# Optimization experiments

Hardware: AMD Instinct MI355X
Metric: run time of the kernel (lower is better)

## Reference

```python
import jax, jax.numpy as jnp
import numpy as np

TILE = 128
NEG = -1e10


def rotate_half(x):
    half = x.shape[-1] // 2
    return jnp.concatenate([-x[..., half:], x[..., :half]], axis=-1)


def setup_inputs() -> dict:
    key = jax.random.key(0)
    ks = jax.random.split(key, 7)
    B, S, E, H, D, K = 1, 4096, 2048, 16, 128, 8
    T = S // TILE
    x = jax.random.normal(ks[0], (B, S, E), jnp.float32)
    wq = jax.random.normal(ks[1], (E, H * D), jnp.float32) * 0.02
    wk = jax.random.normal(ks[2], (E, H * D), jnp.float32) * 0.02
    wv = jax.random.normal(ks[3], (E, H * D), jnp.float32) * 0.02
    wo = jax.random.normal(ks[4], (H * D, E), jnp.float32) * 0.02
    rope_angles = jax.random.uniform(ks[5], (S, D // 2), jnp.float32)
    anchor_indices = jax.random.randint(ks[6], (B, H, T, K), 0, T).astype(jnp.int32)
    return {"x": x, "wq": wq, "wk": wk, "wv": wv, "wo": wo,
            "rope_angles": rope_angles, "anchor_indices": anchor_indices}


def reference(x, wq, wk, wv, wo, rope_angles, anchor_indices):
    B, S, E = x.shape
    D = rope_angles.shape[1] * 2          # head_dim
    H = wq.shape[1] // D                  # num_heads
    T = S // TILE                         # num_tiles
    sm_scale = 1.0 / jnp.sqrt(jnp.float32(D))

    # QKV projections -> [B, H, S, D]
    def proj(w):
        return (x @ w).reshape(B, S, H, D).transpose(0, 2, 1, 3).astype(jnp.float32)
    q, k, v = proj(wq), proj(wk), proj(wv)

    # RoPE (half-split / rotate_half format)
    cos = jnp.cos(rope_angles)[None, None]   # [1,1,S,D/2]
    sin = jnp.sin(rope_angles)[None, None]
    cos_f = jnp.concatenate([cos, cos], axis=-1)
    sin_f = jnp.concatenate([sin, sin], axis=-1)
    q = q * cos_f + rotate_half(q) * sin_f
    k = k * cos_f + rotate_half(k) * sin_f

    # Tile selection: anchor tiles + local (diagonal) tile -> [B,H,T,K+1]
    local = jnp.broadcast_to(jnp.arange(T, dtype=jnp.int32)[None, None, :, None], (B, H, T, 1))
    tile_sel = jnp.concatenate([anchor_indices, local], axis=-1)
    L = tile_sel.shape[-1] * TILE            # sparse_len
    token_idx = tile_sel[..., None] * TILE + jnp.arange(TILE, dtype=jnp.int32)[None, None, None, None, :]
    flat_idx = jnp.clip(token_idx.reshape(B, H, T, L), 0, S - 1)  # [B,H,T,L]

    # Gather selected KV tiles: [B,H,T,L,D]
    def gather(kv):
        return jnp.take_along_axis(kv, flat_idx.reshape(B, H, T * L, 1), axis=2).reshape(B, H, T, L, D)
    k_sp, v_sp = gather(k), gather(v)

    # Block-sparse attention per query tile
    q_t = q.reshape(B, H, T, TILE, D)
    logits = jnp.einsum('bhtqd,bhtkd->bhtqk', q_t, k_sp) * sm_scale
    q_pos = jnp.arange(S).reshape(T, TILE)
    future = flat_idx[:, :, :, None, :] > q_pos[None, None, :, :, None]  # causal mask on gathered keys
    logits = jnp.where(future, NEG, logits)
    w = jax.nn.softmax(logits, axis=-1)
    all_masked = jnp.all(future, axis=-1, keepdims=True)
    w = jnp.where(all_masked, 0.0, w)
    w = jnp.where(jnp.isnan(w), 0.0, w)
    out = jnp.einsum('bhtqk,bhtkd->bhtqd', w, v_sp)

    out = out.reshape(B, H, S, D).transpose(0, 2, 1, 3).reshape(B, S, H * D)
    return out @ wo
```

## Files before the change

kernel.cpp:

```cpp
#include <hip/hip_runtime.h>
#include <stdint.h>

typedef unsigned short u16;
typedef unsigned int u32;

#define S_LEN 4096
#define EMB 2048
#define NH 16
#define HD 128
#define HDTOT 2048
#define T_TILES 32
#define KANCH 8
#define SM_SCALE 0.088388347648318447f

typedef __bf16 bf16x8 __attribute__((ext_vector_type(8)));
typedef float f32x4 __attribute__((ext_vector_type(4)));

typedef const __attribute__((address_space(1))) u32 ga_u32;
typedef __attribute__((address_space(3))) u32 lds_u32;

__device__ __forceinline__ u16 f2bf(float f) {
  u32 b = __builtin_bit_cast(u32, f);
  b = (b + 0x7FFFu + ((b >> 16) & 1u)) >> 16;
  return (u16)b;
}
__device__ __forceinline__ float bf2f(u16 u) {
  return __builtin_bit_cast(float, ((u32)u) << 16);
}
__device__ __forceinline__ f32x4 mfma16(bf16x8 a, bf16x8 b, f32x4 c) {
  return __builtin_amdgcn_mfma_f32_16x16x32_bf16(a, b, c, 0, 0, 0);
}

__global__ __launch_bounds__(256) void k_convert_x(const float* __restrict__ x,
                                                   u16* __restrict__ xb) {
  int i = (blockIdx.x * 256 + threadIdx.x) * 4;
  float4 v = *(const float4*)(x + i);
  ushort4 o;
  o.x = f2bf(v.x); o.y = f2bf(v.y); o.z = f2bf(v.z); o.w = f2bf(v.w);
  *(ushort4*)(xb + i) = o;
}

__global__ __launch_bounds__(256) void k_transpose_w(
    const float* __restrict__ w0, const float* __restrict__ w1,
    const float* __restrict__ w2, const float* __restrict__ w3,
    u16* __restrict__ o0, u16* __restrict__ o1,
    u16* __restrict__ o2, u16* __restrict__ o3) {
  const float* w; u16* o;
  if (blockIdx.z == 0)      { w = w0; o = o0; }
  else if (blockIdx.z == 1) { w = w1; o = o1; }
  else if (blockIdx.z == 2) { w = w2; o = o2; }
  else                      { w = w3; o = o3; }
  __shared__ float tile[64][68];
  int n0 = blockIdx.x * 64, k0 = blockIdx.y * 64;
  int tid = threadIdx.x;
  int r = tid >> 4, cq = (tid & 15) << 2;
  for (int p = 0; p < 4; ++p) {
    float4 v = *(const float4*)(w + (size_t)(k0 + r + p * 16) * EMB + n0 + cq);
    tile[r + p * 16][cq + 0] = v.x;
    tile[r + p * 16][cq + 1] = v.y;
    tile[r + p * 16][cq + 2] = v.z;
    tile[r + p * 16][cq + 3] = v.w;
  }
  __syncthreads();
  for (int p = 0; p < 4; ++p) {
    int rn = r + p * 16;
    ushort4 u;
    u.x = f2bf(tile[cq + 0][rn]);
    u.y = f2bf(tile[cq + 1][rn]);
    u.z = f2bf(tile[cq + 2][rn]);
    u.w = f2bf(tile[cq + 3][rn]);
    *(ushort4*)(o + (size_t)(n0 + rn) * EMB + k0 + cq) = u;
  }
}

__global__ __launch_bounds__(256) void k_transpose_v(const u16* __restrict__ v,
                                                     u16* __restrict__ vt) {
  __shared__ u16 tile[64][72];
  int n0 = blockIdx.x * 64, s0 = blockIdx.y * 64;
  int tid = threadIdx.x;
  int r = tid >> 4, cq = (tid & 15) << 2;
  for (int p = 0; p < 4; ++p) {
    ushort4 u = *(const ushort4*)(v + (size_t)(s0 + r + p * 16) * HDTOT + n0 + cq);
    tile[r + p * 16][cq + 0] = u.x;
    tile[r + p * 16][cq + 1] = u.y;
    tile[r + p * 16][cq + 2] = u.z;
    tile[r + p * 16][cq + 3] = u.w;
  }
  __syncthreads();
  for (int p = 0; p < 4; ++p) {
    int rn = r + p * 16;
    ushort4 o;
    o.x = tile[cq + 0][rn];
    o.y = tile[cq + 1][rn];
    o.z = tile[cq + 2][rn];
    o.w = tile[cq + 3][rn];
    *(ushort4*)(vt + (size_t)(n0 + rn) * S_LEN + s0 + cq) = o;
  }
}

template <bool BF16OUT>
__device__ __forceinline__ void gemm_body(const u16* __restrict__ A,
                                          const u16* __restrict__ Bt,
                                          void* __restrict__ Cv,
                                          int N, int K, int m0, int n0,
                                          u16* As, u16* Bs) {
  const int tid = threadIdx.x;
  const int lane = tid & 63, wave = tid >> 6;
  const int quad = lane >> 4, l16 = lane & 15;
  const int wm = (wave >> 1) * 64, wn = (wave & 1) * 64;
  f32x4 acc[4][4] = {};

  const int flat0 = wave * 1024 + lane * 16;
  for (int kt = 0; kt < K; kt += 32) {
    for (int half = 0; half < 2; ++half) {
      int flat = flat0 + half * 4096;
      int row = flat >> 6, colb = flat & 63;
      const char* ga = (const char*)A + ((size_t)(m0 + row) * K + kt) * 2 + colb;
      const char* gb = (const char*)Bt + ((size_t)(n0 + row) * K + kt) * 2 + colb;
      int loff = wave * 1024 + half * 4096;
      __builtin_amdgcn_global_load_lds((ga_u32*)ga, (lds_u32*)((char*)As + loff), 16, 0, 0);
      __builtin_amdgcn_global_load_lds((ga_u32*)gb, (lds_u32*)((char*)Bs + loff), 16, 0, 0);
    }
    __syncthreads();
    bf16x8 af[4], bfr[4];
    for (int mt = 0; mt < 4; ++mt)
      af[mt] = *(const bf16x8*)(As + (wm + mt * 16 + l16) * 32 + quad * 8);
    for (int nt = 0; nt < 4; ++nt)
      bfr[nt] = *(const bf16x8*)(Bs + (wn + nt * 16 + l16) * 32 + quad * 8);
    for (int mt = 0; mt < 4; ++mt)
      for (int nt = 0; nt < 4; ++nt)
        acc[mt][nt] = mfma16(af[mt], bfr[nt], acc[mt][nt]);
    __syncthreads();
  }
  for (int mt = 0; mt < 4; ++mt) {
    int row = m0 + wm + mt * 16 + quad * 4;
    for (int nt = 0; nt < 4; ++nt) {
      int col = n0 + wn + nt * 16 + l16;
      for (int r = 0; r < 4; ++r) {
        if (BF16OUT)
          ((u16*)Cv)[(size_t)(row + r) * N + col] = f2bf(acc[mt][nt][r]);
        else
          ((float*)Cv)[(size_t)(row + r) * N + col] = acc[mt][nt][r];
      }
    }
  }
}

template <bool BF16OUT>
__global__ __launch_bounds__(256) void k_gemm(const u16* __restrict__ A,
                                              const u16* __restrict__ Bt,
                                              void* __restrict__ Cv,
                                              int N, int K) {
  __shared__ __align__(16) u16 As[128 * 32];
  __shared__ __align__(16) u16 Bs[128 * 32];
  gemm_body<BF16OUT>(A, Bt, Cv, N, K, blockIdx.y * 128, blockIdx.x * 128, As, Bs);
}

__global__ __launch_bounds__(256) void k_gemm_qkv(const u16* __restrict__ A,
                                                  const u16* __restrict__ Bt,
                                                  u16* __restrict__ q,
                                                  u16* __restrict__ k,
                                                  u16* __restrict__ v) {
  __shared__ __align__(16) u16 As[128 * 32];
  __shared__ __align__(16) u16 Bs[128 * 32];
  const int nb = blockIdx.x;
  u16* out = (nb < 16) ? q : ((nb < 32) ? k : v);
  gemm_body<true>(A, Bt + (size_t)((nb >> 4) * 2048) * EMB, out,
                  HDTOT, EMB, blockIdx.y * 128, (nb & 15) * 128, As, Bs);
}

__global__ __launch_bounds__(256) void k_rope(u16* __restrict__ q, u16* __restrict__ k,
                                              const float* __restrict__ ang) {
  int gid = blockIdx.x * 256 + threadIdx.x;
  int s = gid >> 7;
  int h = (gid >> 3) & (NH - 1);
  int dq = (gid & 7) << 3;
  const float* ap = ang + s * 64 + dq;
  float4 a0 = *(const float4*)(ap);
  float4 a1 = *(const float4*)(ap + 4);
  float sn[8], cs[8];
  __sincosf(a0.x, &sn[0], &cs[0]);
  __sincosf(a0.y, &sn[1], &cs[1]);
  __sincosf(a0.z, &sn[2], &cs[2]);
  __sincosf(a0.w, &sn[3], &cs[3]);
  __sincosf(a1.x, &sn[4], &cs[4]);
  __sincosf(a1.y, &sn[5], &cs[5]);
  __sincosf(a1.z, &sn[6], &cs[6]);
  __sincosf(a1.w, &sn[7], &cs[7]);
  size_t base = (size_t)s * HDTOT + h * HD + dq;
  u16* ptrs[2] = {q, k};
#pragma unroll
  for (int a = 0; a < 2; ++a) {
    u16* p = ptrs[a] + base;
    ushort4 x1a = *(const ushort4*)(p);
    ushort4 x1b = *(const ushort4*)(p + 4);
    ushort4 x2a = *(const ushort4*)(p + 64);
    ushort4 x2b = *(const ushort4*)(p + 68);
    u16 v1[8] = {x1a.x, x1a.y, x1a.z, x1a.w, x1b.x, x1b.y, x1b.z, x1b.w};
    u16 v2[8] = {x2a.x, x2a.y, x2a.z, x2a.w, x2b.x, x2b.y, x2b.z, x2b.w};
    u16 o1[8], o2[8];
#pragma unroll
    for (int e = 0; e < 8; ++e) {
      float f1 = bf2f(v1[e]), f2 = bf2f(v2[e]);
      o1[e] = f2bf(f1 * cs[e] - f2 * sn[e]);
      o2[e] = f2bf(f2 * cs[e] + f1 * sn[e]);
    }
    *(ushort4*)(p)      = make_ushort4(o1[0], o1[1], o1[2], o1[3]);
    *(ushort4*)(p + 4)  = make_ushort4(o1[4], o1[5], o1[6], o1[7]);
    *(ushort4*)(p + 64) = make_ushort4(o2[0], o2[1], o2[2], o2[3]);
    *(ushort4*)(p + 68) = make_ushort4(o2[4], o2[5], o2[6], o2[7]);
  }
}

__device__ __forceinline__ bf16x8 ldsfrag(const u16* __restrict__ sbuf, int r, int cb) {
  return *(const bf16x8*)(sbuf + r * 128 + (((cb ^ (r & 15)) << 3)));
}
__device__ __forceinline__ bf16x8 ldsfragV(const u16* __restrict__ sbuf, int r, int cb) {
  return *(const bf16x8*)(sbuf + r * 64 + (((cb ^ (r & 7)) << 3)));
}

__global__ __launch_bounds__(512, 4) void k_attn(const u16* __restrict__ q,
                                                 const u16* __restrict__ k,
                                                 const u16* __restrict__ vt,
                                                 const int* __restrict__ anch,
                                                 u16* __restrict__ out) {
  __shared__ __align__(16) u16 bufK[2][64 * 128];
  __shared__ __align__(16) u16 bufV[2][128 * 64];
  __shared__ int s_tj[KANCH + 1];
  __shared__ int s_nv;
  const int t = T_TILES - 1 - blockIdx.x;
  const int h = blockIdx.y;
  const int tid = threadIdx.x;
  const int lane = tid & 63, wave = tid >> 6;
  const int quad = lane >> 4, l16 = lane & 15;
  const int wq0 = wave * 16;

  int offK[2], offV[2];
#pragma unroll
  for (int p = 0; p < 2; ++p) {
    int krow = (wave * 2 + p) * 4 + (lane >> 4);
    int kcol = ((lane & 15) ^ (krow & 15)) << 3;
    offK[p] = (krow * HDTOT + kcol) * 2;
    int vrow = (wave * 2 + p) * 8 + (lane >> 3);
    int vcol = ((lane & 7) ^ (vrow & 7)) << 3;
    offV[p] = (vrow * S_LEN + vcol) * 2;
  }

  if (tid == 0) {
    int nv = 0;
    for (int j = 0; j < KANCH; ++j) {
      int tj = anch[((h * T_TILES) + t) * KANCH + j];
      if (tj <= t) s_tj[nv++] = tj;
    }
    s_tj[nv++] = t;
    s_nv = nv;
  }

  {
    const char* gq = (const char*)(q + (size_t)(t * 128) * HDTOT + h * HD);
    char* lq = (char*)bufK + wave * 4096;
#pragma unroll
    for (int p = 0; p < 4; ++p) {
      int qrow = (wave * 4 + p) * 4 + (lane >> 4);
      int qcol = ((lane & 15) ^ (qrow & 15)) << 3;
      __builtin_amdgcn_global_load_lds((ga_u32*)(gq + (qrow * HDTOT + qcol) * 2),
                                       (lds_u32*)(lq + p * 1024), 16, 0, 0);
    }
  }
  __syncthreads();

  bf16x8 qf[4];
#pragma unroll
  for (int ks = 0; ks < 4; ++ks)
    qf[ks] = ldsfrag(&bufK[0][0], wq0 + l16, ks * 4 + quad);

  const int nv2 = 2 * s_nv;
  const char* kh = (const char*)(k + h * HD);
  const char* vh = (const char*)(vt + (size_t)(h * HD) * S_LEN);

  __syncthreads();

  {
    int key0 = s_tj[0] * 128;
    const char* gk = kh + (size_t)key0 * (HDTOT * 2);
    const char* gv = vh + (size_t)key0 * 2;
    char* lk = (char*)bufK[0] + wave * 2048;
    char* lv = (char*)bufV[0] + wave * 2048;
#pragma unroll
    for (int p = 0; p < 2; ++p) {
      __builtin_amdgcn_global_load_lds((ga_u32*)(gk + offK[p]),
                                       (lds_u32*)(lk + p * 1024), 16, 0, 0);
      __builtin_amdgcn_global_load_lds((ga_u32*)(gv + offV[p]),
                                       (lds_u32*)(lv + p * 1024), 16, 0, 0);
    }
  }

  f32x4 oacc[8] = {};
  float m_st = -1e30f, l_st = 0.f;

  for (int i = 0; i < nv2; ++i) {
    const int par = i & 1;
    const u16* K_c = bufK[par];
    const u16* V_c = bufV[par];
    const int tj = s_tj[i >> 1];
    const int half = i & 1;
    const bool diag = (tj == t);

    __syncthreads();

    if (i + 1 < nv2) {
      int inx = i + 1;
      int key0 = s_tj[inx >> 1] * 128 + (inx & 1) * 64;
      const char* gk = kh + (size_t)key0 * (HDTOT * 2);
      const char* gv = vh + (size_t)key0 * 2;
      char* lk = (char*)bufK[1 - par] + wave * 2048;
      char* lv = (char*)bufV[1 - par] + wave * 2048;
#pragma unroll
      for (int p = 0; p < 2; ++p) {
        __builtin_amdgcn_global_load_lds((ga_u32*)(gk + offK[p]),
                                         (lds_u32*)(lk + p * 1024), 16, 0, 0);
        __builtin_amdgcn_global_load_lds((ga_u32*)(gv + offV[p]),
                                         (lds_u32*)(lv + p * 1024), 16, 0, 0);
      }
    }

    f32x4 sacc[4] = {};
#pragma unroll
    for (int ks = 0; ks < 4; ++ks)
#pragma unroll
      for (int a = 0; a < 4; ++a) {
        bf16x8 kf = ldsfrag(K_c, a * 16 + l16, ks * 4 + quad);
        sacc[a] = mfma16(kf, qf[ks], sacc[a]);
      }

    u32 pl[4], ph[4];
    float alpha;
    {
      const int qr = wq0 + l16;
      const int kb = half * 64;
      float rmax = -1e30f;
#pragma unroll
      for (int a = 0; a < 4; ++a) {
        f32x4 s4 = sacc[a];
#pragma unroll
        for (int r = 0; r < 4; ++r) {
          float sv = s4[r] * SM_SCALE;
          if (diag && (kb + a * 16 + quad * 4 + r > qr)) sv = -1e30f;
          s4[r] = sv;
          rmax = fmaxf(rmax, sv);
        }
        sacc[a] = s4;
      }
      rmax = fmaxf(rmax, __shfl_xor(rmax, 16));
      rmax = fmaxf(rmax, __shfl_xor(rmax, 32));
      float mnew = fmaxf(m_st, rmax);
      alpha = __expf(m_st - mnew);
      m_st = mnew;
      float rsum = 0.f;
#pragma unroll
      for (int a = 0; a < 4; ++a) {
        f32x4 s4 = sacc[a];
        float p0 = __expf(s4[0] - mnew);
        float p1 = __expf(s4[1] - mnew);
        float p2 = __expf(s4[2] - mnew);
        float p3 = __expf(s4[3] - mnew);
        rsum += (p0 + p1) + (p2 + p3);
        pl[a] = __builtin_amdgcn_perm(__builtin_bit_cast(u32, p1) + 0x8000u,
                                      __builtin_bit_cast(u32, p0) + 0x8000u,
                                      0x07060302u);
        ph[a] = __builtin_amdgcn_perm(__builtin_bit_cast(u32, p3) + 0x8000u,
                                      __builtin_bit_cast(u32, p2) + 0x8000u,
                                      0x07060302u);
      }
      rsum += __shfl_xor(rsum, 16);
      rsum += __shfl_xor(rsum, 32);
      l_st = l_st * alpha + rsum;
    }

    {
      f32x4 av;
#pragma unroll
      for (int r = 0; r < 4; ++r)
        av[r] = __shfl(alpha, (lane & 48) | (quad * 4 + r));
#pragma unroll
      for (int nt = 0; nt < 8; ++nt) {
        f32x4 o4 = oacc[nt];
        o4[0] *= av[0]; o4[1] *= av[1]; o4[2] *= av[2]; o4[3] *= av[3];
        oacc[nt] = o4;
      }
    }

    const int srcA = ((quad & 1) << 5) + l16;
    const int srcB = srcA + 16;
    const int hi = quad >> 1;
#pragma unroll
    for (int c = 0; c < 2; ++c) {
      u32 x0 = __shfl(pl[2 * c], srcA), x1 = __shfl(ph[2 * c], srcA);
      u32 x2 = __shfl(pl[2 * c], srcB), x3 = __shfl(ph[2 * c], srcB);
      u32 y0 = __shfl(pl[2 * c + 1], srcA), y1 = __shfl(ph[2 * c + 1], srcA);
      u32 y2 = __shfl(pl[2 * c + 1], srcB), y3 = __shfl(ph[2 * c + 1], srcB);
      uint4 w;
      w.x = hi ? y0 : x0;
      w.y = hi ? y1 : x1;
      w.z = hi ? y2 : x2;
      w.w = hi ? y3 : x3;
      bf16x8 pa = __builtin_bit_cast(bf16x8, w);
#pragma unroll
      for (int nt = 0; nt < 8; ++nt) {
        bf16x8 vf = ldsfragV(V_c, nt * 16 + l16, c * 4 + quad);
        oacc[nt] = mfma16(pa, vf, oacc[nt]);
      }
    }
  }

  {
    float linv = 1.0f / l_st;
    f32x4 iv;
#pragma unroll
    for (int r = 0; r < 4; ++r)
      iv[r] = __shfl(linv, (lane & 48) | (quad * 4 + r));
#pragma unroll
    for (int r = 0; r < 4; ++r) {
      size_t srow_o = (size_t)(t * 128 + wq0 + quad * 4 + r);
#pragma unroll
      for (int nt = 0; nt < 8; ++nt)
        out[srow_o * HDTOT + h * HD + nt * 16 + l16] = f2bf(oacc[nt][r] * iv[r]);
    }
  }
}

extern "C" void kernel_launch(void* const* d_in, const int* in_sizes, int n_in,
                              void* d_out, int out_size, void* d_ws, size_t ws_size,
                              hipStream_t stream) {
  const float* x   = (const float*)d_in[0];
  const float* wq  = (const float*)d_in[1];
  const float* wk  = (const float*)d_in[2];
  const float* wv  = (const float*)d_in[3];
  const float* wo  = (const float*)d_in[4];
  const float* ang = (const float*)d_in[5];
  const int* anch  = (const int*)d_in[6];

  char* ws = (char*)d_ws;
  const size_t SZ_SE = (size_t)S_LEN * HDTOT * sizeof(u16);
  const size_t SZ_W  = (size_t)EMB * EMB * sizeof(u16);
  u16* xb   = (u16*)(ws);
  u16* qb   = (u16*)(ws + SZ_SE);
  u16* kb   = (u16*)(ws + 2 * SZ_SE);
  u16* vb   = (u16*)(ws + 3 * SZ_SE);
  u16* vtb  = (u16*)(ws + 4 * SZ_SE);
  u16* attn = (u16*)(ws + 5 * SZ_SE);
  u16* wqT  = (u16*)(ws + 6 * SZ_SE);
  u16* wkT  = (u16*)(ws + 6 * SZ_SE + SZ_W);
  u16* wvT  = (u16*)(ws + 6 * SZ_SE + 2 * SZ_W);
  u16* woT  = (u16*)(ws + 6 * SZ_SE + 3 * SZ_W);

  k_convert_x<<<8192, 256, 0, stream>>>(x, xb);
  k_transpose_w<<<dim3(32, 32, 4), 256, 0, stream>>>(wq, wk, wv, wo, wqT, wkT, wvT, woT);
  k_gemm_qkv<<<dim3(48, 32), 256, 0, stream>>>(xb, wqT, qb, kb, vb);
  k_rope<<<2048, 256, 0, stream>>>(qb, kb, ang);
  k_transpose_v<<<dim3(32, 64), 256, 0, stream>>>(vb, vtb);
  k_attn<<<dim3(T_TILES, NH), 512, 0, stream>>>(qb, kb, vtb, anch, attn);
  k_gemm<false><<<dim3(16, 32), 256, 0, stream>>>(attn, woT, d_out, EMB, HDTOT);
}
```

Measured before the change: 400.1 us.

## Replace QKV GEMM with 256x256 direct-to-LDS pipelined kernel and remap attention blocks

Swaps the 128x128 QKV projection GEMM for a 512-thread 256x256-tile kernel. It loads global memory straight into swizzled LDS with global_load_lds and double-buffers the K loop. Each iteration is split into four MFMA phases that overlap the next loads, using explicit waitcnt, barriers and setprio. A grid swizzle groups blocks that share operands for L2 reuse. The attention launch also remaps blocks so heavy and light causal tiles are interleaved across heads, to balance load. The larger tile raises per-tile reuse but leaves only 384 blocks, which may give uneven CU occupancy. The hand-written synchronization is fragile.

```diff
diff --git a/kernel.cpp b/kernel.cpp
--- a/kernel.cpp
+++ b/kernel.cpp
@@ -30,6 +30,11 @@
 __device__ __forceinline__ f32x4 mfma16(bf16x8 a, bf16x8 b, f32x4 c) {
   return __builtin_amdgcn_mfma_f32_16x16x32_bf16(a, b, c, 0, 0, 0);
 }
+
+#define ASM_LGKM0 do { asm volatile("s_waitcnt lgkmcnt(0)" ::: "memory"); \
+                       __builtin_amdgcn_sched_barrier(0); } while (0)
+#define ASM_VMC(n) do { asm volatile("s_waitcnt vmcnt(" #n ")" ::: "memory"); \
+                        __builtin_amdgcn_sched_barrier(0); } while (0)
 
 __global__ __launch_bounds__(256) void k_convert_x(const float* __restrict__ x,
                                                    u16* __restrict__ xb) {
@@ -156,17 +161,152 @@
   gemm_body<BF16OUT>(A, Bt, Cv, N, K, blockIdx.y * 128, blockIdx.x * 128, As, Bs);
 }
 
-__global__ __launch_bounds__(256) void k_gemm_qkv(const u16* __restrict__ A,
-                                                  const u16* __restrict__ Bt,
-                                                  u16* __restrict__ q,
-                                                  u16* __restrict__ k,
-                                                  u16* __restrict__ v) {
-  __shared__ __align__(16) u16 As[128 * 32];
-  __shared__ __align__(16) u16 Bs[128 * 32];
-  const int nb = blockIdx.x;
-  u16* out = (nb < 16) ? q : ((nb < 32) ? k : v);
-  gemm_body<true>(A, Bt + (size_t)((nb >> 4) * 2048) * EMB, out,
-                  HDTOT, EMB, blockIdx.y * 128, (nb & 15) * 128, As, Bs);
+__global__ __launch_bounds__(512, 2) void k_gemm256_qkv(
+    const u16* __restrict__ A, const u16* __restrict__ Bt,
+    u16* __restrict__ q, u16* __restrict__ k, u16* __restrict__ v) {
+  __shared__ __align__(16) u16 lds[65536];
+  int flat = blockIdx.y * 24 + blockIdx.x;
+  flat = (flat & 7) * 48 + (flat >> 3);
+  const int bx = flat % 24, by = flat / 24;
+  const int m0 = by * 256;
+  const int n0g = bx * 256;
+  u16* out = (bx < 8) ? q : ((bx < 16) ? k : v);
+  const int ncol0 = (bx & 7) * 256;
+
+  const int tid = threadIdx.x;
+  const int lane = tid & 63, wave = tid >> 6;
+  const int quad = lane >> 4, l16 = lane & 15;
+  const int wm = wave >> 2, wn = wave & 3;
+  const int sw0 = (quad ^ (l16 & 7)) * 8, sw1 = ((quad ^ (l16 & 7)) ^ 4) * 8;
+
+  size_t soff[2];
+#pragma unroll
+  for (int p = 0; p < 2; ++p) {
+    int fl = p * 8192 + tid * 16;
+    int row = fl >> 7;
+    int gsw = ((fl >> 4) & 7) ^ (row & 7);
+    soff[p] = (size_t)row * 4096 + (size_t)(gsw * 16);
+  }
+  const char* aBase = (const char*)A + (size_t)m0 * 4096;
+  const char* bBase = (const char*)Bt + (size_t)n0g * 4096;
+  const int dstW = wave * 1024;
+
+  auto stA = [&](int buf, int half, int kt) {
+#pragma unroll
+    for (int p = 0; p < 2; ++p)
+      __builtin_amdgcn_global_load_lds(
+          (ga_u32*)(aBase + (size_t)half * 524288 + (size_t)kt * 128 + soff[p]),
+          (lds_u32*)((char*)lds + buf * 32768 + half * 16384 + p * 8192 + dstW),
+          16, 0, 0);
+  };
+  auto stB = [&](int buf, int half, int kt) {
+#pragma unroll
+    for (int p = 0; p < 2; ++p)
+      __builtin_amdgcn_global_load_lds(
+          (ga_u32*)(bBase + (size_t)half * 524288 + (size_t)kt * 128 + soff[p]),
+          (lds_u32*)((char*)lds + 65536 + buf * 32768 + half * 16384 + p * 8192 + dstW),
+          16, 0, 0);
+  };
+  const u16* aRd = lds + wm * 8192 + l16 * 64;
+  const u16* bRd = lds + 32768 + (wn >> 1) * 8192 + ((wn & 1) * 64 + l16) * 64;
+
+  f32x4 acc[8][4] = {};
+
+  stB(0, 0, 0); stA(0, 0, 0); stB(0, 1, 0); stA(0, 1, 0);
+  stB(1, 0, 1); stA(1, 0, 1);
+  ASM_VMC(4);
+  __builtin_amdgcn_s_barrier();
+
+  const int NT = EMB / 64;
+  for (int j = 0; j < NT; ++j) {
+    const int par = j & 1;
+    const u16* aT = aRd + par * 16384;
+    const u16* bT = bRd + par * 16384;
+    bf16x8 af[4][2], blo[2][2], bhi[2][2];
+#pragma unroll
+    for (int m = 0; m < 4; ++m) {
+      af[m][0] = *(const bf16x8*)(aT + m * 1024 + sw0);
+      af[m][1] = *(const bf16x8*)(aT + m * 1024 + sw1);
+    }
+#pragma unroll
+    for (int n = 0; n < 2; ++n) {
+      blo[n][0] = *(const bf16x8*)(bT + n * 1024 + sw0);
+      blo[n][1] = *(const bf16x8*)(bT + n * 1024 + sw1);
+    }
+    if (j + 1 < NT) stB(1 - par, 1, j + 1);
+    __builtin_amdgcn_s_barrier();
+    ASM_LGKM0;
+    __builtin_amdgcn_s_setprio(1);
+#pragma unroll
+    for (int m = 0; m < 4; ++m)
+#pragma unroll
+      for (int n = 0; n < 2; ++n) {
+        acc[m][n] = mfma16(af[m][0], blo[n][0], acc[m][n]);
+        acc[m][n] = mfma16(af[m][1], blo[n][1], acc[m][n]);
+      }
+    __builtin_amdgcn_s_setprio(0);
+    __builtin_amdgcn_s_barrier();
+#pragma unroll
+    for (int n = 0; n < 2; ++n) {
+      bhi[n][0] = *(const bf16x8*)(bT + (n + 2) * 1024 + sw0);
+      bhi[n][1] = *(const bf16x8*)(bT + (n + 2) * 1024 + sw1);
+    }
+    if (j + 1 < NT) stA(1 - par, 1, j + 1);
+    __builtin_amdgcn_s_barrier();
+    ASM_LGKM0;
+    __builtin_amdgcn_s_setprio(1);
+#pragma unroll
+    for (int m = 0; m < 4; ++m)
+#pragma unroll
+      for (int n = 0; n < 2; ++n) {
+        acc[m][n + 2] = mfma16(af[m][0], bhi[n][0], acc[m][n + 2]);
+        acc[m][n + 2] = mfma16(af[m][1], bhi[n][1], acc[m][n + 2]);
+      }
+    __builtin_amdgcn_s_setprio(0);
+    __builtin_amdgcn_s_barrier();
+#pragma unroll
+    for (int m = 0; m < 4; ++m) {
+      af[m][0] = *(const bf16x8*)(aT + (m + 4) * 1024 + sw0);
+      af[m][1] = *(const bf16x8*)(aT + (m + 4) * 1024 + sw1);
+    }
+    if (j + 2 < NT) stB(par, 0, j + 2);
+    __builtin_amdgcn_s_barrier();
+    ASM_LGKM0;
+    __builtin_amdgcn_s_setprio(1);
+#pragma unroll
+    for (int m = 0; m < 4; ++m)
+#pragma unroll
+      for (int n = 0; n < 2; ++n) {
+        acc[m + 4][n + 2] = mfma16(af[m][0], bhi[n][0], acc[m + 4][n + 2]);
+        acc[m + 4][n + 2] = mfma16(af[m][1], bhi[n][1], acc[m + 4][n + 2]);
+      }
+    __builtin_amdgcn_s_setprio(0);
+    __builtin_amdgcn_s_barrier();
+    if (j + 2 < NT) stA(par, 0, j + 2);
+    __builtin_amdgcn_s_barrier();
+    __builtin_amdgcn_s_setprio(1);
+#pragma unroll
+    for (int m = 0; m < 4; ++m)
+#pragma unroll
+      for (int n = 0; n < 2; ++n) {
+        acc[m + 4][n] = mfma16(af[m][0], blo[n][0], acc[m + 4][n]);
+        acc[m + 4][n] = mfma16(af[m][1], blo[n][1], acc[m + 4][n]);
+      }
+    __builtin_amdgcn_s_setprio(0);
+    if (j == NT - 2) { ASM_VMC(0); } else { ASM_VMC(4); }
+    __builtin_amdgcn_s_barrier();
+  }
+#pragma unroll
+  for (int m = 0; m < 8; ++m) {
+    int row = m0 + wm * 128 + m * 16 + quad * 4;
+#pragma unroll
+    for (int n = 0; n < 4; ++n) {
+      int col = ncol0 + wn * 64 + n * 16 + l16;
+#pragma unroll
+      for (int r = 0; r < 4; ++r)
+        out[(size_t)(row + r) * HDTOT + col] = f2bf(acc[m][n][r]);
+    }
+  }
 }
 
 __global__ __launch_bounds__(256) void k_rope(u16* __restrict__ q, u16* __restrict__ k,
@@ -228,8 +368,9 @@
   __shared__ __align__(16) u16 bufV[2][128 * 64];
   __shared__ int s_tj[KANCH + 1];
   __shared__ int s_nv;
-  const int t = T_TILES - 1 - blockIdx.x;
-  const int h = blockIdx.y;
+  const int xx = blockIdx.x, yy = blockIdx.y;
+  const int h = (yy & 7) | ((xx & 1) << 3);
+  const int t = (yy & 8) ? ((xx >> 1) << 1) : (T_TILES - 1 - ((xx >> 1) << 1));
   const int tid = threadIdx.x;
   const int lane = tid & 63, wave = tid >> 6;
   const int quad = lane >> 4, l16 = lane & 15;
@@ -456,7 +597,7 @@
 
   k_convert_x<<<8192, 256, 0, stream>>>(x, xb);
   k_transpose_w<<<dim3(32, 32, 4), 256, 0, stream>>>(wq, wk, wv, wo, wqT, wkT, wvT, woT);
-  k_gemm_qkv<<<dim3(48, 32), 256, 0, stream>>>(xb, wqT, qb, kb, vb);
+  k_gemm256_qkv<<<dim3(24, 16), 512, 0, stream>>>(xb, wqT, qb, kb, vb);
   k_rope<<<2048, 256, 0, stream>>>(qb, kb, ang);
   k_transpose_v<<<dim3(32, 64), 256, 0, stream>>>(vb, vtb);
   k_attn<<<dim3(T_TILES, NH), 512, 0, stream>>>(qb, kb, vtb, anch, attn);
```

Measured after the change: 383.6 us. 1.04x faster.
